# Performance work log

Hardware: AMD Instinct MI355X
Metric: run time of the kernel (lower is better)

Reference implementation:

```python
import jax, jax.numpy as jnp
import numpy as np

N_NODES = 100000


def gcn_conv(x, src, dst, W, b):
    # PyG GCNConv: linear transform first, then symmetric-normalized aggregation.
    h = x @ W  # [N, out]
    ones = jnp.ones(dst.shape[0], dtype=x.dtype)
    deg = jax.ops.segment_sum(ones, dst, num_segments=N_NODES)  # in-degree incl. self-loops
    dinv = jnp.where(deg > 0, jax.lax.rsqrt(deg), 0.0)
    norm = dinv[src] * dinv[dst]  # [E]
    msg = h[src] * norm[:, None]  # gather + scale
    out = jax.ops.segment_sum(msg, dst, num_segments=N_NODES)  # scatter-add
    return out + b


def add_self_loops(edge_index):
    loops = jnp.arange(N_NODES, dtype=edge_index.dtype)
    src = jnp.concatenate([edge_index[0], loops])
    dst = jnp.concatenate([edge_index[1], loops])
    return src, dst


def setup_inputs() -> dict:
    key = jax.random.key(0)
    k1, k2, k3, k4 = jax.random.split(key, 4)
    N, F, H, C, E = N_NODES, 512, 16, 40, 3200000
    x = jax.random.normal(k1, (N, F), dtype=jnp.float32)
    edge_index = jax.random.randint(k2, (2, E), 0, N, dtype=jnp.int64)
    W1 = jax.random.normal(k3, (F, H), dtype=jnp.float32) * (1.0 / np.sqrt(F))
    b1 = jnp.zeros((H,), dtype=jnp.float32)
    W2 = jax.random.normal(k4, (H, C), dtype=jnp.float32) * (1.0 / np.sqrt(H))
    b2 = jnp.zeros((C,), dtype=jnp.float32)
    return {"x": x, "edge_index": edge_index, "W1": W1, "b1": b1, "W2": W2, "b2": b2}


def reference(x, edge_index, W1, b1, W2, b2):
    src, dst = add_self_loops(edge_index)
    h = gcn_conv(x, src, dst, W1, b1)
    h = jax.nn.relu(h)
    logits = gcn_conv(h, src, dst, W2, b2)
    return jax.nn.log_softmax(logits, axis=1), logits
```

## Files before the change

### kernel.cpp

```cpp
#include <hip/hip_runtime.h>
#include <hip/hip_bf16.h>
#include <math.h>

#define N_NODES 100000
#define F_IN 512
#define H_DIM 16
#define C_DIM 40

#define BSHIFT 9
#define BNODES 512
#define NBUCK 196
#define CHUNK 8192
#define SRC_MASK 0x1FFFF


__global__ void __launch_bounds__(256) bhist_kernel(const int* __restrict__ dst,
                                                    int* __restrict__ BC, int E) {
    __shared__ int cnt[NBUCK];
    int start = blockIdx.x * CHUNK;
    int end = start + CHUNK < E ? start + CHUNK : E;
    for (int i = threadIdx.x; i < NBUCK; i += 256) cnt[i] = 0;
    __syncthreads();
    for (int i = start + threadIdx.x; i < end; i += 256)
        atomicAdd(&cnt[dst[i] >> BSHIFT], 1);
    __syncthreads();
    for (int i = threadIdx.x; i < NBUCK; i += 256) {
        int c = cnt[i];
        if (c) atomicAdd(&BC[i], c);
    }
}


__global__ void __launch_bounds__(256) bscan_kernel(const int* __restrict__ BC,
                                                    int* __restrict__ BO,
                                                    int* __restrict__ cursor,
                                                    int* __restrict__ R, int E, int N) {
    __shared__ int buf[2][256];
    int tid = threadIdx.x;
    int v = (tid < NBUCK) ? BC[tid] : 0;
    int cur = 0;
    buf[0][tid] = v;
    __syncthreads();
    for (int off = 1; off < 256; off <<= 1) {
        int t = buf[cur][tid] + ((tid >= off) ? buf[cur][tid - off] : 0);
        cur ^= 1;
        buf[cur][tid] = t;
        __syncthreads();
    }
    int excl = buf[cur][tid] - v;
    if (tid <= NBUCK) {
        BO[tid] = excl;
        if (tid < NBUCK) cursor[tid] = excl;
    }
    if (tid == 0) R[N] = E;
}


__global__ void __launch_bounds__(256) partition_kernel(const int* __restrict__ src,
                                                        const int* __restrict__ dst,
                                                        int* __restrict__ cursor,
                                                        int* __restrict__ packed, int E) {
    __shared__ int cnt[NBUCK];
    __shared__ int base[NBUCK];
    int start = blockIdx.x * CHUNK;
    int end = start + CHUNK < E ? start + CHUNK : E;
    for (int i = threadIdx.x; i < NBUCK; i += 256) cnt[i] = 0;
    __syncthreads();
    for (int i = start + threadIdx.x; i < end; i += 256)
        atomicAdd(&cnt[dst[i] >> BSHIFT], 1);
    __syncthreads();
    for (int i = threadIdx.x; i < NBUCK; i += 256) {
        int c = cnt[i];
        base[i] = c ? atomicAdd(&cursor[i], c) : 0;
        cnt[i] = 0;
    }
    __syncthreads();
    for (int i = start + threadIdx.x; i < end; i += 256) {
        int d = dst[i];
        int b = d >> BSHIFT;
        int p = base[b] + atomicAdd(&cnt[b], 1);
        packed[p] = ((d & (BNODES - 1)) << 17) | src[i];
    }
}


__global__ void __launch_bounds__(512) sort2_kernel(const int* __restrict__ BO,
                                                    const int* __restrict__ packed,
                                                    int* __restrict__ R,
                                                    float* __restrict__ dinv,
                                                    int* __restrict__ eidx, int N) {
    __shared__ int cnt[BNODES];
    __shared__ int buf[2][BNODES];
    int b = blockIdx.x;
    int tid = threadIdx.x;
    int lo = BO[b], hi = BO[b + 1];
    cnt[tid] = 0;
    __syncthreads();
    for (int e = lo + tid; e < hi; e += 512)
        atomicAdd(&cnt[packed[e] >> 17], 1);
    __syncthreads();
    int deg = cnt[tid];
    int cur = 0;
    buf[0][tid] = deg;
    __syncthreads();
    for (int off = 1; off < 512; off <<= 1) {
        int t = buf[cur][tid] + ((tid >= off) ? buf[cur][tid - off] : 0);
        cur ^= 1;
        buf[cur][tid] = t;
        __syncthreads();
    }
    int excl = lo + buf[cur][tid] - deg;
    int n = (b << BSHIFT) + tid;
    if (n < N) {
        R[n] = excl;
        dinv[n] = rsqrtf((float)(deg + 1));
    }
    cnt[tid] = excl;
    __syncthreads();
    for (int e = lo + tid; e < hi; e += 512) {
        int p = packed[e];
        int pos = atomicAdd(&cnt[p >> 17], 1);
        eidx[pos] = p & SRC_MASK;
    }
}


#define G1_ISSUE(BUF, KC)                                            \
    {                                                                \
        _Pragma("unroll")                                            \
        for (int p = 0; p < 4; ++p) BUF[p] = xr[(KC) * 4 + p];       \
    }

#define G1_COMPUTE(BUF, KC)                                          \
    {                                                                \
        const float4* Wk = (const float4*)(W1 + (KC) * 16 * H_DIM);  \
        const float* xf = (const float*)BUF;                         \
        _Pragma("unroll")                                            \
        for (int j = 0; j < 16; ++j) {                               \
            float s = xf[j];                                         \
            _Pragma("unroll")                                        \
            for (int p = 0; p < 4; ++p) {                            \
                float4 wv = Wk[j * 4 + p];                           \
                acc[4 * p + 0] += s * wv.x;                          \
                acc[4 * p + 1] += s * wv.y;                          \
                acc[4 * p + 2] += s * wv.z;                          \
                acc[4 * p + 3] += s * wv.w;                          \
            }                                                        \
        }                                                            \
    }

__global__ void __launch_bounds__(64) gemm1_kernel(const float* __restrict__ x,
                                                   const float* __restrict__ W1,
                                                   const float* __restrict__ dinv,
                                                   float* __restrict__ g1, int N) {
    int row = blockIdx.x * 64 + threadIdx.x;
    int cr = row < N ? row : N - 1;
    const float4* xr = (const float4*)(x + (size_t)cr * F_IN);

    float4 bufA[4], bufB[4];
    float acc[H_DIM];
#pragma unroll
    for (int k = 0; k < H_DIM; k++) acc[k] = 0.0f;

    G1_ISSUE(bufA, 0);
#pragma unroll
    for (int kc = 0; kc < F_IN / 16; kc += 2) {
        G1_ISSUE(bufB, kc + 1);
        G1_COMPUTE(bufA, kc);
        if (kc + 2 < F_IN / 16) G1_ISSUE(bufA, kc + 2);
        G1_COMPUTE(bufB, kc + 1);
    }

    if (row < N) {
        float di = dinv[row];
        float4* o = (float4*)(g1 + (size_t)row * H_DIM);
#pragma unroll
        for (int p = 0; p < 4; p++)
            o[p] = make_float4(acc[4 * p] * di, acc[4 * p + 1] * di,
                               acc[4 * p + 2] * di, acc[4 * p + 3] * di);
    }
}


__global__ void __launch_bounds__(256) agg1_kernel(const int* __restrict__ R,
                                                   const int* __restrict__ eidx,
                                                   const float* __restrict__ g1,
                                                   const float* __restrict__ dinv,
                                                   const float* __restrict__ b1,
                                                   float* __restrict__ g2, int N) {
    int t = blockIdx.x * 256 + threadIdx.x;
    int n = t >> 4;
    if (n >= N) return;
    int k = t & 15;
    int lo = R[n], hi = R[n + 1];
    float sum = g1[t];
    int e = lo;
    for (; e + 8 <= hi; e += 8) {
        int s[8];
        float v[8];
#pragma unroll
        for (int u = 0; u < 8; u++) s[u] = eidx[e + u];
#pragma unroll
        for (int u = 0; u < 8; u++) v[u] = g1[s[u] * H_DIM + k];
#pragma unroll
        for (int u = 0; u < 8; u++) sum += v[u];
    }
    for (; e < hi; ++e) sum += g1[eidx[e] * H_DIM + k];
    float di = dinv[n];
    g2[t] = di * fmaxf(di * sum + b1[k], 0.0f);
}

__global__ void __launch_bounds__(256) agg2_kernel(const int* __restrict__ R,
                                                   const int* __restrict__ eidx,
                                                   const float* __restrict__ g2,
                                                   float* __restrict__ s2, int N) {
    int t = blockIdx.x * 256 + threadIdx.x;
    int n = t >> 4;
    if (n >= N) return;
    int k = t & 15;
    int lo = R[n], hi = R[n + 1];
    float sum = g2[t];
    int e = lo;
    for (; e + 8 <= hi; e += 8) {
        int s[8];
        float v[8];
#pragma unroll
        for (int u = 0; u < 8; u++) s[u] = eidx[e + u];
#pragma unroll
        for (int u = 0; u < 8; u++) v[u] = g2[s[u] * H_DIM + k];
#pragma unroll
        for (int u = 0; u < 8; u++) sum += v[u];
    }
    for (; e < hi; ++e) sum += g2[eidx[e] * H_DIM + k];
    s2[t] = sum;
}


__global__ void __launch_bounds__(256) final_kernel(const float* __restrict__ s2,
                                                    const float* __restrict__ dinv,
                                                    const float* __restrict__ W2,
                                                    const float* __restrict__ b2,
                                                    float* __restrict__ out, int N) {
    __shared__ float w2s[H_DIM * C_DIM];
    __shared__ float b2s[C_DIM];
    __shared__ float stage[256 * 41];
    for (int i = threadIdx.x; i < H_DIM * C_DIM; i += 256) w2s[i] = W2[i];
    if (threadIdx.x < C_DIM) b2s[threadIdx.x] = b2[threadIdx.x];
    __syncthreads();
    int n = blockIdx.x * 256 + threadIdx.x;
    int cn = n < N ? n : 0;
    float di = dinv[cn];
    float v[H_DIM];
    const float4* sv = (const float4*)(s2 + (size_t)cn * H_DIM);
#pragma unroll
    for (int p = 0; p < 4; p++) {
        float4 t = sv[p];
        v[4 * p] = di * t.x; v[4 * p + 1] = di * t.y;
        v[4 * p + 2] = di * t.z; v[4 * p + 3] = di * t.w;
    }
    float lg[C_DIM];
    float m = -1e30f;
    for (int c = 0; c < C_DIM; c++) {
        float a = b2s[c];
#pragma unroll
        for (int k = 0; k < H_DIM; k++) a += v[k] * w2s[k * C_DIM + c];
        lg[c] = a;
        m = fmaxf(m, a);
    }
    float ssum = 0.0f;
    for (int c = 0; c < C_DIM; c++) ssum += __expf(lg[c] - m);
    float lse = m + __logf(ssum);

    size_t base = (size_t)blockIdx.x * 256 * C_DIM;
    size_t lim = (size_t)N * C_DIM;
    for (int c = 0; c < C_DIM; c++) stage[threadIdx.x * 41 + c] = lg[c] - lse;
    __syncthreads();
    for (int i = threadIdx.x; i < 256 * C_DIM; i += 256) {
        int nn = i / C_DIM, c = i - nn * C_DIM;
        size_t g = base + i;
        if (g < lim) out[g] = stage[nn * 41 + c];
    }
    __syncthreads();
    for (int c = 0; c < C_DIM; c++) stage[threadIdx.x * 41 + c] = lg[c];
    __syncthreads();
    for (int i = threadIdx.x; i < 256 * C_DIM; i += 256) {
        int nn = i / C_DIM, c = i - nn * C_DIM;
        size_t g = base + i;
        if (g < lim) out[lim + g] = stage[nn * 41 + c];
    }
}


extern "C" void kernel_launch(void* const* d_in, const int* in_sizes, int n_in,
                              void* d_out, int out_size, void* d_ws, size_t ws_size,
                              hipStream_t stream) {
    const float* x  = (const float*)d_in[0];
    const int* ei   = (const int*)d_in[1];
    const float* W1 = (const float*)d_in[2];
    const float* b1 = (const float*)d_in[3];
    const float* W2 = (const float*)d_in[4];
    const float* b2 = (const float*)d_in[5];
    float* out = (float*)d_out;

    const int N = N_NODES;
    const int E = in_sizes[1] / 2;
    const int* src = ei;
    const int* dst = ei + E;

    int* R      = (int*)d_ws;
    int* BC     = R + 100016;
    int* BO     = BC + 512;
    int* cursor = BO + 256;
    float* dinv = (float*)(cursor + 256);
    int* eidx   = (int*)(dinv + 100016);
    int* packed = eidx + E;
    float* g1   = (float*)packed;
    float* g2   = g1 + 16 * N;
    float* s2   = g1;

    const int NB = (N + 255) / 256;
    const int NCH = (E + CHUNK - 1) / CHUNK;

    hipMemsetAsync(BC, 0, NBUCK * sizeof(int), stream);
    bhist_kernel<<<NCH, 256, 0, stream>>>(dst, BC, E);
    bscan_kernel<<<1, 256, 0, stream>>>(BC, BO, cursor, R, E, N);
    partition_kernel<<<NCH, 256, 0, stream>>>(src, dst, cursor, packed, E);
    sort2_kernel<<<NBUCK, 512, 0, stream>>>(BO, packed, R, dinv, eidx, N);

    gemm1_kernel<<<(N + 63) / 64, 64, 0, stream>>>(x, W1, dinv, g1, N);
    agg1_kernel<<<(N * 16 + 255) / 256, 256, 0, stream>>>(R, eidx, g1, dinv, b1, g2, N);
    agg2_kernel<<<(N * 16 + 255) / 256, 256, 0, stream>>>(R, eidx, g2, s2, N);
    final_kernel<<<NB, 256, 0, stream>>>(s2, dinv, W2, b2, out, N);
}
```

Baseline: 534.9 us.

## Split gemm1 along K into four partial blocks plus reduction kernel

The first-layer GEMM now splits the 512-wide reduction dimension into four segments, each handled by its own block that writes partial sums to a workspace. A new reduction kernel adds the four partials and applies the dinv scaling. The goal is to launch four times more blocks (about 1563 row blocks before, 64 threads each) so more waves are in flight to hide the latency of streaming x. The cost is an extra kernel launch and writing then reading 4x16 floats per node of partial results.

```diff
diff --git a/kernel.cpp b/kernel.cpp
--- a/kernel.cpp
+++ b/kernel.cpp
@@ -12,6 +12,9 @@
 #define NBUCK 196
 #define CHUNK 8192
 #define SRC_MASK 0x1FFFF
+
+#define KSPLIT 4
+#define KSEG (F_IN / KSPLIT)
 
 
 __global__ void __launch_bounds__(256) bhist_kernel(const int* __restrict__ dst,
@@ -133,7 +136,7 @@
 
 #define G1_COMPUTE(BUF, KC)                                          \
     {                                                                \
-        const float4* Wk = (const float4*)(W1 + (KC) * 16 * H_DIM);  \
+        const float4* Wk = (const float4*)(Wb + (KC) * 16 * H_DIM);  \
         const float* xf = (const float*)BUF;                         \
         _Pragma("unroll")                                            \
         for (int j = 0; j < 16; ++j) {                               \
@@ -149,13 +152,16 @@
         }                                                            \
     }
 
-__global__ void __launch_bounds__(64) gemm1_kernel(const float* __restrict__ x,
-                                                   const float* __restrict__ W1,
-                                                   const float* __restrict__ dinv,
-                                                   float* __restrict__ g1, int N) {
-    int row = blockIdx.x * 64 + threadIdx.x;
+__global__ void __launch_bounds__(64) gemm1p_kernel(const float* __restrict__ x,
+                                                    const float* __restrict__ W1,
+                                                    float* __restrict__ part, int N) {
+    int bid = blockIdx.x;
+    int ks = bid & (KSPLIT - 1);
+    int rb = bid >> 2;
+    int row = rb * 64 + threadIdx.x;
     int cr = row < N ? row : N - 1;
-    const float4* xr = (const float4*)(x + (size_t)cr * F_IN);
+    const float4* xr = (const float4*)(x + (size_t)cr * F_IN + ks * KSEG);
+    const float* Wb = W1 + ks * KSEG * H_DIM;
 
     float4 bufA[4], bufB[4];
     float acc[H_DIM];
@@ -164,21 +170,38 @@
 
     G1_ISSUE(bufA, 0);
 #pragma unroll
-    for (int kc = 0; kc < F_IN / 16; kc += 2) {
+    for (int kc = 0; kc < KSEG / 16; kc += 2) {
         G1_ISSUE(bufB, kc + 1);
         G1_COMPUTE(bufA, kc);
-        if (kc + 2 < F_IN / 16) G1_ISSUE(bufA, kc + 2);
+        if (kc + 2 < KSEG / 16) G1_ISSUE(bufA, kc + 2);
         G1_COMPUTE(bufB, kc + 1);
     }
 
     if (row < N) {
-        float di = dinv[row];
-        float4* o = (float4*)(g1 + (size_t)row * H_DIM);
+        float4* o = (float4*)(part + (size_t)ks * N * H_DIM + (size_t)row * H_DIM);
 #pragma unroll
         for (int p = 0; p < 4; p++)
-            o[p] = make_float4(acc[4 * p] * di, acc[4 * p + 1] * di,
-                               acc[4 * p + 2] * di, acc[4 * p + 3] * di);
-    }
+            o[p] = make_float4(acc[4 * p], acc[4 * p + 1], acc[4 * p + 2], acc[4 * p + 3]);
+    }
+}
+
+
+__global__ void __launch_bounds__(256) g1red_kernel(const float* __restrict__ part,
+                                                    const float* __restrict__ dinv,
+                                                    float* __restrict__ g1, int N) {
+    int t = blockIdx.x * 256 + threadIdx.x;
+    int total = N * H_DIM / 4;
+    if (t >= total) return;
+    const float4* p = (const float4*)part;
+    float4 a = p[t];
+    float4 b = p[t + (size_t)total];
+    float4 c = p[t + (size_t)2 * total];
+    float4 d = p[t + (size_t)3 * total];
+    float di = dinv[t >> 2];
+    ((float4*)g1)[t] = make_float4(di * (((a.x + b.x) + c.x) + d.x),
+                                   di * (((a.y + b.y) + c.y) + d.y),
+                                   di * (((a.z + b.z) + c.z) + d.z),
+                                   di * (((a.w + b.w) + c.w) + d.w));
 }
 
 
@@ -317,9 +340,11 @@
     float* g1   = (float*)packed;
     float* g2   = g1 + 16 * N;
     float* s2   = g1;
+    float* part = g2 + 16 * N;
 
     const int NB = (N + 255) / 256;
     const int NCH = (E + CHUNK - 1) / CHUNK;
+    const int NRB = (N + 63) / 64;
 
     hipMemsetAsync(BC, 0, NBUCK * sizeof(int), stream);
     bhist_kernel<<<NCH, 256, 0, stream>>>(dst, BC, E);
@@ -327,7 +352,8 @@
     partition_kernel<<<NCH, 256, 0, stream>>>(src, dst, cursor, packed, E);
     sort2_kernel<<<NBUCK, 512, 0, stream>>>(BO, packed, R, dinv, eidx, N);
 
-    gemm1_kernel<<<(N + 63) / 64, 64, 0, stream>>>(x, W1, dinv, g1, N);
+    gemm1p_kernel<<<NRB * KSPLIT, 64, 0, stream>>>(x, W1, part, N);
+    g1red_kernel<<<(N * H_DIM / 4 + 255) / 256, 256, 0, stream>>>(part, dinv, g1, N);
     agg1_kernel<<<(N * 16 + 255) / 256, 256, 0, stream>>>(R, eidx, g1, dinv, b1, g2, N);
     agg2_kernel<<<(N * 16 + 255) / 256, 256, 0, stream>>>(R, eidx, g2, s2, N);
     final_kernel<<<NB, 256, 0, stream>>>(s2, dinv, W2, b2, out, N);
```

After: 531.4 us. No clear change (-0.7%).
